# Optimization experiments

Measured on AMD Instinct MI355X. Metric: run time of the kernel, lower is better.

Reference implementation:

```python
import jax, jax.numpy as jnp
import numpy as np

B, N, C = 128, 36, 1024
K_NB = 16            # neighbors per node (top-k, includes loop)
KERNEL = 8           # number of Gaussian kernels
OUT = 1024           # out_dim; per-kernel out = OUT // KERNEL
PI = np.float32(np.pi)


def setup_inputs() -> dict:
    key = jax.random.key(0)
    ks = jax.random.split(key, 9)
    node_feats = jax.random.normal(ks[0], (B, N, C), dtype=jnp.float32)
    node_centre = jax.random.uniform(ks[1], (B, N, 2), dtype=jnp.float32)
    neighbor_idx = jax.random.randint(ks[2], (B * N, K_NB), 0, B * N, dtype=jnp.int32)
    graph_weights = jax.random.uniform(ks[3], (B * N * K_NB, 1), dtype=jnp.float32)
    # Gaussian kernel params (per reset_parameters)
    mean_rho = jax.random.uniform(ks[4], (1, KERNEL), dtype=jnp.float32)
    mean_theta = jax.random.uniform(ks[5], (1, KERNEL), minval=-PI, maxval=PI, dtype=jnp.float32)
    precision_rho = jax.random.uniform(ks[6], (1, KERNEL), minval=0.5, maxval=1.0, dtype=jnp.float32)
    precision_theta = jax.random.uniform(ks[7], (1, KERNEL), minval=0.5, maxval=1.0, dtype=jnp.float32)
    # per-kernel Linear(node_dim, out_dim//kernel, bias=False), stacked: [K, d_out_k, C]
    conv_w = jax.random.normal(ks[8], (KERNEL, OUT // KERNEL, C), dtype=jnp.float32) * (1.0 / np.sqrt(C))
    return {
        "node_feats": node_feats,
        "node_centre": node_centre,
        "neighbor_idx": neighbor_idx,
        "graph_weights": graph_weights,
        "mean_rho": mean_rho,
        "mean_theta": mean_theta,
        "precision_rho": precision_rho,
        "precision_theta": precision_theta,
        "conv_w": conv_w,
    }


def _forward(node_feats, node_centre, graph_weights,
             mean_rho, mean_theta, precision_rho, precision_theta,
             conv_w, neighbor_idx):
    b, n, c = node_feats.shape
    bn = b * n
    # pseudo polar coordinates per edge: centre_i - centre_j
    centre = node_centre.reshape(bn, 2)                       # [BN, 2]
    diff = centre[:, None, :] - centre[neighbor_idx]          # [BN, K_nb, 2]
    coord_x = diff[..., 0].reshape(-1)                        # [E]
    coord_y = diff[..., 1].reshape(-1)
    rho = jnp.sqrt(coord_x ** 2 + coord_y ** 2)
    theta = jnp.arctan2(coord_x, coord_y)
    # Gaussian mixture membership weights over KERNEL kernels
    w_rho = jnp.exp(-0.5 * (rho[:, None] - mean_rho) ** 2 / (1e-14 + precision_rho ** 2))
    first_angle = jnp.abs(theta[:, None] - mean_theta)
    second_angle = jnp.abs(2.0 * PI - first_angle)
    w_theta = jnp.exp(-0.5 * jnp.minimum(first_angle, second_angle) ** 2 / (1e-14 + precision_theta ** 2))
    weights = w_rho * w_theta                                  # [E, KERNEL]
    weights = jnp.where(jnp.isnan(weights), 0.0, weights)
    weights = weights / jnp.sum(weights, axis=1, keepdims=True)
    # combine with graph edge weights
    edge_w = graph_weights * weights                           # [E, KERNEL]
    edge_w = edge_w.reshape(bn, K_NB, KERNEL).transpose(0, 2, 1)  # [BN, K, K_nb]
    # gather neighbor features and weighted aggregate (bmm)
    nbr = node_feats.reshape(bn, c)[neighbor_idx]              # [BN, K_nb, C]
    agg = jnp.einsum('ekn,enc->ekc', edge_w, nbr)              # [BN, KERNEL, C]
    agg = agg.reshape(b, n, KERNEL, c)
    # per-kernel linear then concat over kernel dim
    out = jnp.einsum('bnkc,kdc->bnkd', agg, conv_w)            # [B, N, KERNEL, OUT//KERNEL]
    out = out.reshape(b, n, -1)                                # [B, N, OUT]
    return jax.nn.relu(out)


def reference(node_feats, node_centre, neighbor_idx, graph_weights,
              mean_rho, mean_theta, precision_rho, precision_theta, conv_w):
    return _forward(node_feats, node_centre, graph_weights,
                    mean_rho, mean_theta, precision_rho, precision_theta,
                    conv_w, neighbor_idx)
```

## Files before the change

kernel.cpp:

```cpp
#include <hip/hip_runtime.h>
#include <hip/hip_bf16.h>
#include <stdint.h>

#define B_DIM   128
#define N_DIM   36
#define C_DIM   1024
#define KNB     16
#define NKER    8
#define OUTD    1024
#define BN_NODES (B_DIM * N_DIM)
#define E_EDGES  (BN_NODES * KNB)
#define PI_F 3.14159265358979323846f

#define TM 64
#define TN 128
#define BK 64
#define KIT (C_DIM / BK)
#define CLP 136
#define A_OFF(p) ((p) * TM * BK)
#define B_OFF(p) (2 * TM * BK + (p) * TN * BK)

typedef __attribute__((ext_vector_type(8))) short bf16x8;
typedef __attribute__((ext_vector_type(4))) float floatx4;

struct alignas(8) U16x4 { unsigned short x, y, z, w; };

__device__ __forceinline__ unsigned short f2bf(float f) {
  union { float f; uint32_t u; } v; v.f = f;
  uint32_t u = v.u;
  return (unsigned short)((u + 0x7fffu + ((u >> 16) & 1u)) >> 16);
}
__device__ __forceinline__ float bf2f_lo(uint32_t pair) {
  union { uint32_t u; float f; } v; v.u = pair << 16;
  return v.f;
}
__device__ __forceinline__ float bf2f_hi(uint32_t pair) {
  union { uint32_t u; float f; } v; v.u = pair & 0xffff0000u;
  return v.f;
}

__device__ __forceinline__ void gload16(const void* g, void* l) {
  __builtin_amdgcn_global_load_lds((__attribute__((address_space(1))) void*)(g),
                                   (__attribute__((address_space(3))) void*)(l),
                                   16, 0, 0);
}

__global__ __launch_bounds__(256)
void cast_kernel(const float* __restrict__ feats,
                 const float* __restrict__ cw,
                 unsigned short* __restrict__ fb,
                 unsigned short* __restrict__ wb)
{
  const int NF4 = (BN_NODES * C_DIM) / 4;
  const int NW4 = (C_DIM * OUTD) / 4;
  int tid = blockIdx.x * 256 + threadIdx.x;
  if (tid < NF4) {
    float4 v = ((const float4*)feats)[tid];
    U16x4 o = { f2bf(v.x), f2bf(v.y), f2bf(v.z), f2bf(v.w) };
    ((U16x4*)fb)[tid] = o;
  } else {
    int t = tid - NF4;
    if (t < NW4) {
      float4 v = ((const float4*)cw)[t];
      U16x4 o = { f2bf(v.x), f2bf(v.y), f2bf(v.z), f2bf(v.w) };
      ((U16x4*)wb)[t] = o;
    }
  }
}

__global__ __launch_bounds__(256)
void gemm_bt(const unsigned short* __restrict__ A,
             const unsigned short* __restrict__ Bt,
             unsigned short* __restrict__ D)
{
  __shared__ unsigned short smem[2 * TM * BK + 2 * TN * BK];

  const int tid  = threadIdx.x;
  const int lane = tid & 63;
  const int wave = tid >> 6;
  const int wm   = wave >> 1;
  const int wn   = wave & 1;
  const int row0 = blockIdx.x * TM;
  const int col0 = blockIdx.y * TN;

  const int q  = lane >> 4;
  const int lr = lane & 15;

  floatx4 acc[2][4] = {};

  int offA[2], offB[4];
#pragma unroll
  for (int i = 0; i < 2; ++i) {
    int c = tid + 256 * i, row = c >> 3, qc = c & 7;
    offA[i] = (row0 + row) * C_DIM + (qc ^ (row & 7)) * 8;
  }
#pragma unroll
  for (int i = 0; i < 4; ++i) {
    int c = tid + 256 * i, row = c >> 3, qc = c & 7;
    offB[i] = (col0 + row) * C_DIM + (qc ^ (row & 7)) * 8;
  }

#define DMA(T, P) do {                                                       \
    _Pragma("unroll") for (int i = 0; i < 2; ++i)                            \
      gload16(A + offA[i] + (T) * BK,                                        \
              &smem[A_OFF(P) + (tid + 256 * i) * 8]);                        \
    _Pragma("unroll") for (int i = 0; i < 4; ++i)                            \
      gload16(Bt + offB[i] + (T) * BK,                                       \
              &smem[B_OFF(P) + (tid + 256 * i) * 8]);                        \
  } while (0)

  DMA(0, 0);

  for (int t = 0; t < KIT; ++t) {
    const int p = t & 1;
    __syncthreads();
    if (t + 1 < KIT) DMA(t + 1, 1 - p);

    const int aBase = A_OFF(p);
    const int bBase = B_OFF(p);
#pragma unroll
    for (int kc = 0; kc < 2; ++kc) {
      const int sc = ((kc * 4 + q) ^ (lr & 7)) * 8;
      bf16x8 af[2], bfr[4];
#pragma unroll
      for (int i = 0; i < 2; ++i)
        af[i]  = *(const bf16x8*)&smem[aBase + (wm * 32 + i * 16 + lr) * BK + sc];
#pragma unroll
      for (int j = 0; j < 4; ++j)
        bfr[j] = *(const bf16x8*)&smem[bBase + (wn * 64 + j * 16 + lr) * BK + sc];
#pragma unroll
      for (int i = 0; i < 2; ++i)
#pragma unroll
        for (int j = 0; j < 4; ++j)
          acc[i][j] = __builtin_amdgcn_mfma_f32_16x16x32_bf16(
              af[i], bfr[j], acc[i][j], 0, 0, 0);
    }
  }
#undef DMA

  __syncthreads();
#pragma unroll
  for (int i = 0; i < 2; ++i)
#pragma unroll
    for (int j = 0; j < 4; ++j)
#pragma unroll
      for (int r = 0; r < 4; ++r)
        smem[(wm * 32 + i * 16 + q * 4 + r) * CLP + wn * 64 + j * 16 + lr] =
            f2bf(acc[i][j][r]);
  __syncthreads();
#pragma unroll
  for (int i = 0; i < 4; ++i) {
    int c = tid + 256 * i;
    int row = c >> 4, qc = c & 15;
    *(uint4*)&D[(size_t)(row0 + row) * OUTD + col0 + qc * 8] =
        *(const uint4*)&smem[row * CLP + qc * 8];
  }
}

__global__ __launch_bounds__(256)
void agg_fused(const unsigned short* __restrict__ proj,
               const float* __restrict__ centre,
               const int*   __restrict__ nbr,
               const float* __restrict__ gw,
               const float* __restrict__ mrho,
               const float* __restrict__ mth,
               const float* __restrict__ prho,
               const float* __restrict__ pth,
               float* __restrict__ out)
{
  __shared__ int   idx[2][KNB];
  __shared__ float nxy[2][KNB][2];
  __shared__ float cxy[2][2];
  __shared__ float wk[2][KNB][NKER];
  __shared__ float scl[2][KNB];
  __shared__ float ew[2][NKER][KNB];

  const int n0   = blockIdx.x * 2;
  const int t    = threadIdx.x;
  const int half = t >> 7;
  const int u    = t & 127;

  if (t < 32) {
    int h = t >> 4, j = t & 15;
    int m = nbr[(n0 + h) * KNB + j];
    idx[h][j] = m;
    nxy[h][j][0] = centre[2 * m];
    nxy[h][j][1] = centre[2 * m + 1];
  } else if (t < 34) {
    int h = t - 32;
    cxy[h][0] = centre[2 * (n0 + h)];
    cxy[h][1] = centre[2 * (n0 + h) + 1];
  }
  __syncthreads();

  {
    int j = u >> 3, k = u & 7;
    float cx = cxy[half][0] - nxy[half][j][0];
    float cy = cxy[half][1] - nxy[half][j][1];
    float rho   = sqrtf(cx * cx + cy * cy);
    float theta = atan2f(cx, cy);
    float dr = rho - mrho[k];
    float pr = prho[k];
    float w_r = expf(-0.5f * dr * dr / (1e-14f + pr * pr));
    float fa = fabsf(theta - mth[k]);
    float sa = fabsf(2.0f * PI_F - fa);
    float mm = fminf(fa, sa);
    float pt = pth[k];
    float w_t = expf(-0.5f * mm * mm / (1e-14f + pt * pt));
    float ww = w_r * w_t;
    wk[half][j][k] = (ww != ww) ? 0.f : ww;
  }
  __syncthreads();

  if (u < KNB) {
    float s = 0.f;
#pragma unroll
    for (int k = 0; k < NKER; ++k) s += wk[half][u][k];
    scl[half][u] = gw[(n0 + half) * KNB + u] / s;
  }
  __syncthreads();

  {
    int j = u >> 3, k = u & 7;
    ew[half][k][j] = wk[half][j][k] * scl[half][j];
  }
  __syncthreads();

  const int n = n0 + half;
  const int k = u >> 4;
  float a[8] = {0.f, 0.f, 0.f, 0.f, 0.f, 0.f, 0.f, 0.f};
#pragma unroll
  for (int j = 0; j < KNB; ++j) {
    float wv = ew[half][k][j];
    uint4 v = *(const uint4*)&proj[(size_t)idx[half][j] * OUTD + u * 8];
    a[0] += wv * bf2f_lo(v.x);  a[1] += wv * bf2f_hi(v.x);
    a[2] += wv * bf2f_lo(v.y);  a[3] += wv * bf2f_hi(v.y);
    a[4] += wv * bf2f_lo(v.z);  a[5] += wv * bf2f_hi(v.z);
    a[6] += wv * bf2f_lo(v.w);  a[7] += wv * bf2f_hi(v.w);
  }
  float4 r0, r1;
  r0.x = fmaxf(a[0], 0.f); r0.y = fmaxf(a[1], 0.f);
  r0.z = fmaxf(a[2], 0.f); r0.w = fmaxf(a[3], 0.f);
  r1.x = fmaxf(a[4], 0.f); r1.y = fmaxf(a[5], 0.f);
  r1.z = fmaxf(a[6], 0.f); r1.w = fmaxf(a[7], 0.f);
  float* o = out + (size_t)n * OUTD + u * 8;
  *(float4*)(o)     = r0;
  *(float4*)(o + 4) = r1;
}

extern "C" void kernel_launch(void* const* d_in, const int* in_sizes, int n_in,
                              void* d_out, int out_size, void* d_ws, size_t ws_size,
                              hipStream_t stream)
{
  const float* feats  = (const float*)d_in[0];
  const float* centre = (const float*)d_in[1];
  const int*   nbr    = (const int*)  d_in[2];
  const float* gw     = (const float*)d_in[3];
  const float* mrho   = (const float*)d_in[4];
  const float* mth    = (const float*)d_in[5];
  const float* prho   = (const float*)d_in[6];
  const float* pth    = (const float*)d_in[7];
  const float* cw     = (const float*)d_in[8];
  float* out = (float*)d_out;

  char* ws = (char*)d_ws;
  unsigned short* fb   = (unsigned short*)(ws);
  unsigned short* wb   = (unsigned short*)(ws + 9437184);
  unsigned short* proj = (unsigned short*)(ws + 11534336);

  cast_kernel<<<dim3(((BN_NODES * C_DIM) / 4 + (C_DIM * OUTD) / 4) / 256),
                dim3(256), 0, stream>>>(feats, cw, fb, wb);
  gemm_bt<<<dim3(BN_NODES / TM, OUTD / TN), dim3(256), 0, stream>>>(fb, wb, proj);
  agg_fused<<<dim3(BN_NODES / 2), dim3(256), 0, stream>>>(
      proj, centre, nbr, gw, mrho, mth, prho, pth, out);
}
```

Measured before the change: 123.4 us.

## Move edge-weight computation into cast kernel and retile gather for locality

Edge Gaussian weights are now computed per edge inside the cast kernel, one thread per edge, and written to a workspace buffer. This removes the serialized shared-memory phases and barriers from the aggregation kernel. The aggregation kernel is rewritten so each block handles 8 nodes by a 256-channel slice, with a block-index swizzle meant to improve cache reuse of gathered projection rows. The cost is an extra global round trip for the edge weights and a larger cast-kernel grid.

```diff
diff --git a/kernel.cpp b/kernel.cpp
--- a/kernel.cpp
+++ b/kernel.cpp
@@ -46,10 +46,18 @@
 }
 
 __global__ __launch_bounds__(256)
-void cast_kernel(const float* __restrict__ feats,
-                 const float* __restrict__ cw,
-                 unsigned short* __restrict__ fb,
-                 unsigned short* __restrict__ wb)
+void cast_ew_kernel(const float* __restrict__ feats,
+                    const float* __restrict__ cw,
+                    const float* __restrict__ centre,
+                    const int*   __restrict__ nbr,
+                    const float* __restrict__ gw,
+                    const float* __restrict__ mrho,
+                    const float* __restrict__ mth,
+                    const float* __restrict__ prho,
+                    const float* __restrict__ pth,
+                    unsigned short* __restrict__ fb,
+                    unsigned short* __restrict__ wb,
+                    float* __restrict__ ewg)
 {
   const int NF4 = (BN_NODES * C_DIM) / 4;
   const int NW4 = (C_DIM * OUTD) / 4;
@@ -64,6 +72,37 @@
       float4 v = ((const float4*)cw)[t];
       U16x4 o = { f2bf(v.x), f2bf(v.y), f2bf(v.z), f2bf(v.w) };
       ((U16x4*)wb)[t] = o;
+    } else {
+      int e = t - NW4;
+      if (e < E_EDGES) {
+        int n = e >> 4;
+        int m = nbr[e];
+        float cx = centre[2 * n]     - centre[2 * m];
+        float cy = centre[2 * n + 1] - centre[2 * m + 1];
+        float rho   = sqrtf(cx * cx + cy * cy);
+        float theta = atan2f(cx, cy);
+        float wk[NKER];
+        float s = 0.f;
+#pragma unroll
+        for (int k = 0; k < NKER; ++k) {
+          float dr = rho - mrho[k];
+          float pr = prho[k];
+          float w_r = expf(-0.5f * dr * dr / (1e-14f + pr * pr));
+          float fa = fabsf(theta - mth[k]);
+          float sa = fabsf(2.0f * PI_F - fa);
+          float mm = fminf(fa, sa);
+          float pt = pth[k];
+          float w_t = expf(-0.5f * mm * mm / (1e-14f + pt * pt));
+          float ww = w_r * w_t;
+          wk[k] = (ww != ww) ? 0.f : ww;
+          s += wk[k];
+        }
+        float scale = gw[e] / s;
+        int j = e & 15;
+#pragma unroll
+        for (int k = 0; k < NKER; ++k)
+          ewg[(size_t)n * (NKER * KNB) + k * KNB + j] = wk[k] * scale;
+      }
     }
   }
 }
@@ -158,92 +197,51 @@
 }
 
 __global__ __launch_bounds__(256)
-void agg_fused(const unsigned short* __restrict__ proj,
-               const float* __restrict__ centre,
-               const int*   __restrict__ nbr,
-               const float* __restrict__ gw,
-               const float* __restrict__ mrho,
-               const float* __restrict__ mth,
-               const float* __restrict__ prho,
-               const float* __restrict__ pth,
-               float* __restrict__ out)
-{
-  __shared__ int   idx[2][KNB];
-  __shared__ float nxy[2][KNB][2];
-  __shared__ float cxy[2][2];
-  __shared__ float wk[2][KNB][NKER];
-  __shared__ float scl[2][KNB];
-  __shared__ float ew[2][NKER][KNB];
-
-  const int n0   = blockIdx.x * 2;
-  const int t    = threadIdx.x;
-  const int half = t >> 7;
-  const int u    = t & 127;
-
-  if (t < 32) {
-    int h = t >> 4, j = t & 15;
-    int m = nbr[(n0 + h) * KNB + j];
-    idx[h][j] = m;
-    nxy[h][j][0] = centre[2 * m];
-    nxy[h][j][1] = centre[2 * m + 1];
-  } else if (t < 34) {
-    int h = t - 32;
-    cxy[h][0] = centre[2 * (n0 + h)];
-    cxy[h][1] = centre[2 * (n0 + h) + 1];
+void agg_gather(const unsigned short* __restrict__ proj,
+                const int*   __restrict__ nbr,
+                const float* __restrict__ ewg,
+                float* __restrict__ out)
+{
+  __shared__ int   idx[8][KNB];
+  __shared__ float ewl[8][2][KNB];
+
+  const int bid = blockIdx.x;
+  const int x   = bid & 7;
+  const int s   = x >> 1;
+  const int g   = ((bid >> 3) << 1) | (x & 1);
+  const int n0  = g * 8;
+  const int t   = threadIdx.x;
+
+  if (t < 128)
+    idx[t >> 4][t & 15] = nbr[(n0 + (t >> 4)) * KNB + (t & 15)];
+  {
+    int a = t >> 5, r = t & 31;
+    ewl[a][r >> 4][r & 15] = ewg[(size_t)(n0 + a) * (NKER * KNB) + s * 32 + r];
   }
   __syncthreads();
 
-  {
-    int j = u >> 3, k = u & 7;
-    float cx = cxy[half][0] - nxy[half][j][0];
-    float cy = cxy[half][1] - nxy[half][j][1];
-    float rho   = sqrtf(cx * cx + cy * cy);
-    float theta = atan2f(cx, cy);
-    float dr = rho - mrho[k];
-    float pr = prho[k];
-    float w_r = expf(-0.5f * dr * dr / (1e-14f + pr * pr));
-    float fa = fabsf(theta - mth[k]);
-    float sa = fabsf(2.0f * PI_F - fa);
-    float mm = fminf(fa, sa);
-    float pt = pth[k];
-    float w_t = expf(-0.5f * mm * mm / (1e-14f + pt * pt));
-    float ww = w_r * w_t;
-    wk[half][j][k] = (ww != ww) ? 0.f : ww;
-  }
-  __syncthreads();
-
-  if (u < KNB) {
-    float s = 0.f;
-#pragma unroll
-    for (int k = 0; k < NKER; ++k) s += wk[half][u][k];
-    scl[half][u] = gw[(n0 + half) * KNB + u] / s;
-  }
-  __syncthreads();
-
-  {
-    int j = u >> 3, k = u & 7;
-    ew[half][k][j] = wk[half][j][k] * scl[half][j];
-  }
-  __syncthreads();
-
-  const int n = n0 + half;
-  const int k = u >> 4;
-  float a[8] = {0.f, 0.f, 0.f, 0.f, 0.f, 0.f, 0.f, 0.f};
+  const int a   = t >> 5;
+  const int cu  = t & 31;
+  const int kk  = cu >> 4;
+  const int n   = n0 + a;
+  const int ch0 = s * 256 + cu * 8;
+
+  float acc[8] = {0.f, 0.f, 0.f, 0.f, 0.f, 0.f, 0.f, 0.f};
 #pragma unroll
   for (int j = 0; j < KNB; ++j) {
-    float wv = ew[half][k][j];
-    uint4 v = *(const uint4*)&proj[(size_t)idx[half][j] * OUTD + u * 8];
-    a[0] += wv * bf2f_lo(v.x);  a[1] += wv * bf2f_hi(v.x);
-    a[2] += wv * bf2f_lo(v.y);  a[3] += wv * bf2f_hi(v.y);
-    a[4] += wv * bf2f_lo(v.z);  a[5] += wv * bf2f_hi(v.z);
-    a[6] += wv * bf2f_lo(v.w);  a[7] += wv * bf2f_hi(v.w);
+    float wv = ewl[a][kk][j];
+    uint4 v = *(const uint4*)&proj[(size_t)idx[a][j] * OUTD + ch0];
+    acc[0] += wv * bf2f_lo(v.x);  acc[1] += wv * bf2f_hi(v.x);
+    acc[2] += wv * bf2f_lo(v.y);  acc[3] += wv * bf2f_hi(v.y);
+    acc[4] += wv * bf2f_lo(v.z);  acc[5] += wv * bf2f_hi(v.z);
+    acc[6] += wv * bf2f_lo(v.w);  acc[7] += wv * bf2f_hi(v.w);
   }
   float4 r0, r1;
-  r0.x = fmaxf(a[0], 0.f); r0.y = fmaxf(a[1], 0.f);
-  r0.z = fmaxf(a[2], 0.f); r0.w = fmaxf(a[3], 0.f);
-  r1.x = fmaxf(a[4], 0.f); r1.y = fmaxf(a[5], 0.f);
-  r1.z = fmaxf(a[6], 0.f); r1.w = fmaxf(a[7], 0.f);
-  float* o = out + (size_t)n * OUTD + u * 8;
+  r0.x = fmaxf(acc[0], 0.f); r0.y = fmaxf(acc[1], 0.f);
+  r0.z = fmaxf(acc[2], 0.f); r0.w = fmaxf(acc[3], 0.f);
+  r1.x = fmaxf(acc[4], 0.f); r1.y = fmaxf(acc[5], 0.f);
+  r1.z = fmaxf(acc[6], 0.f); r1.w = fmaxf(acc[7], 0.f);
+  float* o = out + (size_t)n * OUTD + ch0;
   *(float4*)(o)     = r0;
   *(float4*)(o + 4) = r1;
 }
@@ -267,10 +265,13 @@
   unsigned short* fb   = (unsigned short*)(ws);
   unsigned short* wb   = (unsigned short*)(ws + 9437184);
   unsigned short* proj = (unsigned short*)(ws + 11534336);
-
-  cast_kernel<<<dim3(((BN_NODES * C_DIM) / 4 + (C_DIM * OUTD) / 4) / 256),
-                dim3(256), 0, stream>>>(feats, cw, fb, wb);
+  float*          ewg  = (float*)         (ws + 20971520);
+
+  const int NF4 = (BN_NODES * C_DIM) / 4;
+  const int NW4 = (C_DIM * OUTD) / 4;
+  const int EWB = (E_EDGES + 255) / 256;
+  cast_ew_kernel<<<dim3((NF4 + NW4) / 256 + EWB), dim3(256), 0, stream>>>(
+      feats, cw, centre, nbr, gw, mrho, mth, prho, pth, fb, wb, ewg);
   gemm_bt<<<dim3(BN_NODES / TM, OUTD / TN), dim3(256), 0, stream>>>(fb, wb, proj);
-  agg_fused<<<dim3(BN_NODES / 2), dim3(256), 0, stream>>>(
-      proj, centre, nbr, gw, mrho, mth, prho, pth, out);
-}
+  agg_gather<<<dim3(BN_NODES / 2), dim3(256), 0, stream>>>(proj, nbr, ewg, out);
+}
```

Result: no change. 122.3 us (-0.9%).
